# Kernel tuning notes

Measured on AMD Instinct MI355X. Metric: run time of the kernel, lower is better.

Reference implementation:

```python
import jax, jax.numpy as jnp
import numpy as np

N_NODES = 100000
N_EDGES = 3200000
IN_F = 256
OUT_F = 256


def setup_inputs() -> dict:
    key = jax.random.key(0)
    k1, k2, k3, k4, k5 = jax.random.split(key, 5)
    input_ = jax.random.normal(k1, (N_NODES, IN_F), dtype=jnp.float32)
    edge_src = jax.random.randint(k2, (N_EDGES,), 0, N_NODES, dtype=jnp.int64)
    edge_dst = jax.random.randint(k3, (N_EDGES,), 0, N_NODES, dtype=jnp.int64)
    edge_val = jax.random.uniform(k4, (N_EDGES,), dtype=jnp.float32)
    stdv = 1.0 / np.sqrt(OUT_F)
    weight = jax.random.uniform(k5, (IN_F, OUT_F), dtype=jnp.float32,
                                minval=-stdv, maxval=stdv)
    return {"input_": input_, "edge_src": edge_src, "edge_dst": edge_dst,
            "edge_val": edge_val, "weight": weight}


def reference(input_, edge_src, edge_dst, edge_val, weight):
    # neighbor = spmm(adj, input_): adj in COO form (dst, src, val)
    gathered = edge_val[:, None] * input_[edge_src]          # [E, F]
    neighbor = jax.ops.segment_sum(gathered, edge_dst,
                                   num_segments=N_NODES)     # [N, F]
    ft_input = input_ @ weight                               # [N, O]
    ft_neighbor = neighbor @ weight                          # [N, O]
    return jnp.concatenate([ft_input, ft_neighbor], axis=1)  # [N, 2*O]
```

## Files before the change

kernel.cpp:

```cpp
#include <hip/hip_runtime.h>
#include <hip/hip_fp16.h>

#define N_NODES 100000
#define N_EDGES 3200000
#define F 256

#define BM 64
#define BN 256
#define BK 32

#define MAX_DEG 80
#define INIT_NB ((N_NODES + 255) / 256)
#define EDGE_NB4 (N_EDGES / 1024)
#define GEMM_NB ((N_NODES + BM - 1) / BM)
#define FUSED_NB (GEMM_NB + EDGE_NB4)

typedef __attribute__((ext_vector_type(8))) short short8;
typedef __attribute__((ext_vector_type(4))) float f32x4;

__device__ inline unsigned short f2bf(float f) {
    unsigned int u = __float_as_uint(f);
    unsigned int r = (u + 0x7fffu + ((u >> 16) & 1u)) >> 16;
    return (unsigned short)r;
}

__device__ inline float bf2f(unsigned short b) {
    return __uint_as_float(((unsigned int)b) << 16);
}

__device__ inline unsigned int pack_rec(int src, float val) {
    __half h = __float2half(val);
    unsigned short hb = *reinterpret_cast<unsigned short*>(&h);
    return ((unsigned int)src << 15) | (unsigned int)hb;
}

__device__ inline int rec_src(unsigned int p) { return (int)(p >> 15); }

__device__ inline float rec_val(unsigned int p) {
    unsigned short hb = (unsigned short)(p & 0x7FFFu);
    __half h = *reinterpret_cast<__half*>(&hb);
    return __half2float(h);
}

__global__ __launch_bounds__(256)
void init_kernel(const float* __restrict__ W, unsigned short* __restrict__ Wt,
                 int* __restrict__ counts) {
    const int idx = blockIdx.x * 256 + threadIdx.x;
    if (idx < N_NODES) counts[idx] = 0;
    if (idx < 256 * 256) {
        const int n = idx >> 8;
        const int k = idx & 255;
        Wt[n * 256 + k] = f2bf(W[k * 256 + n]);
    }
}

__global__ __launch_bounds__(256, 3)
void gemm_bucket_kernel(const float* __restrict__ A,
                        const unsigned short* __restrict__ Wt,
                        float* __restrict__ out,
                        unsigned short* __restrict__ ftb,
                        const int* __restrict__ src,
                        const int* __restrict__ dst,
                        const float* __restrict__ val,
                        int* __restrict__ counts,
                        unsigned int* __restrict__ recs)
{
    const int bid = blockIdx.x;

    if (bid % 3 != 0) {
        const int ebid = 2 * (bid / 3) + (bid % 3) - 1;
        const int e0 = (ebid * 256 + threadIdx.x) * 4;
        const int4   s = *(const int4*)(src + e0);
        const int4   d = *(const int4*)(dst + e0);
        const float4 v = *(const float4*)(val + e0);
        const int r0 = atomicAdd(&counts[d.x], 1);
        const int r1 = atomicAdd(&counts[d.y], 1);
        const int r2 = atomicAdd(&counts[d.z], 1);
        const int r3 = atomicAdd(&counts[d.w], 1);
        if (r0 < MAX_DEG) recs[d.x * MAX_DEG + r0] = pack_rec(s.x, v.x);
        if (r1 < MAX_DEG) recs[d.y * MAX_DEG + r1] = pack_rec(s.y, v.y);
        if (r2 < MAX_DEG) recs[d.z * MAX_DEG + r2] = pack_rec(s.z, v.z);
        if (r3 < MAX_DEG) recs[d.w * MAX_DEG + r3] = pack_rec(s.w, v.w);
        return;
    }

    const int tid   = threadIdx.x;
    const int lane  = tid & 63;
    const int wave  = tid >> 6;
    const int waveM = wave >> 1;
    const int waveN = wave & 1;
    const int rowBase = (bid / 3) * BM;

    const int quad = lane >> 4;
    const int l16  = lane & 15;

    f32x4 acc[2][8];
#pragma unroll
    for (int i = 0; i < 2; i++)
#pragma unroll
        for (int j = 0; j < 8; j++) acc[i][j] = (f32x4)0.0f;

    const int row0 = rowBase + waveM * 32 + l16;
    const int row1 = row0 + 16;
    const bool ok0 = row0 < N_NODES;
    const bool ok1 = row1 < N_NODES;
    const float* pa0 = A + (size_t)row0 * 256 + quad * 8;
    const float* pa1 = A + (size_t)row1 * 256 + quad * 8;
    const unsigned short* pb = Wt + (size_t)(waveN * 128 + l16) * 256 + quad * 8;

    for (int kt = 0; kt < 8; kt++) {
        const int k0 = kt * BK;

        short8 af[2];
#pragma unroll
        for (int i = 0; i < 2; i++) {
            const float* pa = (i == 0) ? pa0 : pa1;
            const bool ok = (i == 0) ? ok0 : ok1;
            short8 av;
            if (ok) {
                const float4 f0 = *(const float4*)(pa + k0);
                const float4 f1 = *(const float4*)(pa + k0 + 4);
                av[0] = (short)f2bf(f0.x); av[1] = (short)f2bf(f0.y);
                av[2] = (short)f2bf(f0.z); av[3] = (short)f2bf(f0.w);
                av[4] = (short)f2bf(f1.x); av[5] = (short)f2bf(f1.y);
                av[6] = (short)f2bf(f1.z); av[7] = (short)f2bf(f1.w);
            } else {
                av = (short8)0;
            }
            af[i] = av;
        }

        short8 bfr[8];
#pragma unroll
        for (int j = 0; j < 8; j++)
            bfr[j] = *(const short8*)(pb + (size_t)(j * 16) * 256 + k0);

#pragma unroll
        for (int i = 0; i < 2; i++)
#pragma unroll
            for (int j = 0; j < 8; j++)
                acc[i][j] = __builtin_amdgcn_mfma_f32_16x16x32_bf16(
                    bfr[j], af[i], acc[i][j], 0, 0, 0);
    }

#pragma unroll
    for (int i = 0; i < 2; i++) {
        const int row = rowBase + waveM * 32 + i * 16 + l16;
        if (row < N_NODES) {
#pragma unroll
            for (int j = 0; j < 8; j++) {
                const int col = waveN * 128 + j * 16 + quad * 4;
                f32x4 v = acc[i][j];
                *(f32x4*)(out + (size_t)row * 512 + col) = v;
                unsigned int p0 = ((unsigned int)f2bf(v[1]) << 16) | f2bf(v[0]);
                unsigned int p1 = ((unsigned int)f2bf(v[3]) << 16) | f2bf(v[2]);
                *(uint2*)(ftb + (size_t)row * 256 + col) = make_uint2(p0, p1);
            }
        }
    }
}

__global__ __launch_bounds__(256)
void gather_kernel(const int* __restrict__ counts,
                   const unsigned int* __restrict__ recs,
                   const unsigned short* __restrict__ ftb,
                   float* __restrict__ out)
{
    const int n = blockIdx.x * 4 + (threadIdx.x >> 6);
    if (n >= N_NODES) return;
    const int lane = threadIdx.x & 63;

    int len = counts[n];
    if (len > MAX_DEG) len = MAX_DEG;
    const unsigned int* rp = recs + (size_t)n * MAX_DEG;

    float ax = 0.f, ay = 0.f, az = 0.f, aw = 0.f;

    int e = 0;

    if (e + 7 < len) {
        unsigned int r[8];
#pragma unroll
        for (int q = 0; q < 8; q++) r[q] = rp[e + q];
        while (true) {
            const int en = e + 8;
            const bool moreN = (en + 7 < len);
            unsigned int rn[8];
            if (moreN) {
#pragma unroll
                for (int q = 0; q < 8; q++) rn[q] = rp[en + q];
            }
            ushort4 u[8];
#pragma unroll
            for (int q = 0; q < 8; q++)
                u[q] = *(const ushort4*)(ftb + (size_t)rec_src(r[q]) * 256 + lane * 4);
#pragma unroll
            for (int q = 0; q < 8; q++) {
                const float v = rec_val(r[q]);
                ax += v * bf2f(u[q].x); ay += v * bf2f(u[q].y);
                az += v * bf2f(u[q].z); aw += v * bf2f(u[q].w);
            }
            e = en;
            if (!moreN) break;
#pragma unroll
            for (int q = 0; q < 8; q++) r[q] = rn[q];
        }
    }

    for (; e + 3 < len; e += 4) {
        unsigned int r0 = rp[e];
        unsigned int r1 = rp[e + 1];
        unsigned int r2 = rp[e + 2];
        unsigned int r3 = rp[e + 3];
        ushort4 u0 = *(const ushort4*)(ftb + (size_t)rec_src(r0) * 256 + lane * 4);
        ushort4 u1 = *(const ushort4*)(ftb + (size_t)rec_src(r1) * 256 + lane * 4);
        ushort4 u2 = *(const ushort4*)(ftb + (size_t)rec_src(r2) * 256 + lane * 4);
        ushort4 u3 = *(const ushort4*)(ftb + (size_t)rec_src(r3) * 256 + lane * 4);
        const float v0 = rec_val(r0);
        const float v1 = rec_val(r1);
        const float v2 = rec_val(r2);
        const float v3 = rec_val(r3);
        ax += v0 * bf2f(u0.x); ay += v0 * bf2f(u0.y);
        az += v0 * bf2f(u0.z); aw += v0 * bf2f(u0.w);
        ax += v1 * bf2f(u1.x); ay += v1 * bf2f(u1.y);
        az += v1 * bf2f(u1.z); aw += v1 * bf2f(u1.w);
        ax += v2 * bf2f(u2.x); ay += v2 * bf2f(u2.y);
        az += v2 * bf2f(u2.z); aw += v2 * bf2f(u2.w);
        ax += v3 * bf2f(u3.x); ay += v3 * bf2f(u3.y);
        az += v3 * bf2f(u3.z); aw += v3 * bf2f(u3.w);
    }
    for (; e < len; e++) {
        unsigned int r0 = rp[e];
        ushort4 u0 = *(const ushort4*)(ftb + (size_t)rec_src(r0) * 256 + lane * 4);
        const float v0 = rec_val(r0);
        ax += v0 * bf2f(u0.x); ay += v0 * bf2f(u0.y);
        az += v0 * bf2f(u0.z); aw += v0 * bf2f(u0.w);
    }

    float4 res = make_float4(ax, ay, az, aw);
    *(float4*)(out + (size_t)n * 512 + 256 + lane * 4) = res;
}

extern "C" void kernel_launch(void* const* d_in, const int* in_sizes, int n_in,
                              void* d_out, int out_size, void* d_ws, size_t ws_size,
                              hipStream_t stream)
{
    const float* input = (const float*)d_in[0];
    const int*   esrc  = (const int*)d_in[1];
    const int*   edst  = (const int*)d_in[2];
    const float* eval  = (const float*)d_in[3];
    const float* W     = (const float*)d_in[4];
    float* out = (float*)d_out;

    char* ws = (char*)d_ws;
    unsigned short* Wt  = (unsigned short*)(ws);
    int* counts         = (int*)(ws + 131072);
    unsigned int* recs  = (unsigned int*)(ws + 532480);
    unsigned short* ftb = (unsigned short*)(ws + 32532480);

    init_kernel<<<INIT_NB, 256, 0, stream>>>(W, Wt, counts);

    gemm_bucket_kernel<<<FUSED_NB, 256, 0, stream>>>(
        input, Wt, out, ftb, esrc, edst, eval, counts, recs);

    gather_kernel<<<(N_NODES + 3) / 4, 256, 0, stream>>>(counts, recs, ftb, out);
}
```

Before: 710.2 us.

## Stage converted A tile through double-buffered LDS shared across waves

Each thread now loads and converts one 8-element slice of the A tile to bf16 once and writes it into a double-buffered shared-memory tile. All waves then read their MFMA operands from LDS, where before each wave pair redundantly loaded and converted the same rows from global memory. The next k-tile is prefetched while the current one is consumed, at the cost of a block barrier per k-step and 8KB of LDS, which may lower occupancy for the fused edge-bucketing blocks.

```diff
diff --git a/kernel.cpp b/kernel.cpp
--- a/kernel.cpp
+++ b/kernel.cpp
@@ -65,6 +65,8 @@
                         int* __restrict__ counts,
                         unsigned int* __restrict__ recs)
 {
+    __shared__ unsigned short As[2][BM * BK];
+
     const int bid = blockIdx.x;
 
     if (bid % 3 != 0) {
@@ -91,49 +93,56 @@
     const int waveN = wave & 1;
     const int rowBase = (bid / 3) * BM;
 
+    const int sr = tid >> 2;
+    const int sk = (tid & 3) * 8;
     const int quad = lane >> 4;
     const int l16  = lane & 15;
 
+    const int  grow = rowBase + sr;
+    const bool gok  = grow < N_NODES;
+    const float* pa = A + (size_t)grow * 256 + sk;
+    const unsigned short* pb = Wt + (size_t)(waveN * 128 + l16) * 256 + quad * 8;
+
     f32x4 acc[2][8];
 #pragma unroll
     for (int i = 0; i < 2; i++)
 #pragma unroll
         for (int j = 0; j < 8; j++) acc[i][j] = (f32x4)0.0f;
 
-    const int row0 = rowBase + waveM * 32 + l16;
-    const int row1 = row0 + 16;
-    const bool ok0 = row0 < N_NODES;
-    const bool ok1 = row1 < N_NODES;
-    const float* pa0 = A + (size_t)row0 * 256 + quad * 8;
-    const float* pa1 = A + (size_t)row1 * 256 + quad * 8;
-    const unsigned short* pb = Wt + (size_t)(waveN * 128 + l16) * 256 + quad * 8;
-
+#define STAGE_A(buf, kt)                                                     \
+    {                                                                        \
+        short8 av;                                                           \
+        if (gok) {                                                           \
+            const float4 f0 = *(const float4*)(pa + (kt) * BK);              \
+            const float4 f1 = *(const float4*)(pa + (kt) * BK + 4);          \
+            av[0] = (short)f2bf(f0.x); av[1] = (short)f2bf(f0.y);            \
+            av[2] = (short)f2bf(f0.z); av[3] = (short)f2bf(f0.w);            \
+            av[4] = (short)f2bf(f1.x); av[5] = (short)f2bf(f1.y);            \
+            av[6] = (short)f2bf(f1.z); av[7] = (short)f2bf(f1.w);            \
+        } else {                                                             \
+            av = (short8)0;                                                  \
+        }                                                                    \
+        *(short8*)(&As[buf][sr * BK + sk]) = av;                             \
+    }
+
+    STAGE_A(0, 0);
+    __syncthreads();
+
+#pragma unroll
     for (int kt = 0; kt < 8; kt++) {
+        const int cur = kt & 1;
+        if (kt < 7) STAGE_A(cur ^ 1, kt + 1);
+
         const int k0 = kt * BK;
-
-        short8 af[2];
-#pragma unroll
-        for (int i = 0; i < 2; i++) {
-            const float* pa = (i == 0) ? pa0 : pa1;
-            const bool ok = (i == 0) ? ok0 : ok1;
-            short8 av;
-            if (ok) {
-                const float4 f0 = *(const float4*)(pa + k0);
-                const float4 f1 = *(const float4*)(pa + k0 + 4);
-                av[0] = (short)f2bf(f0.x); av[1] = (short)f2bf(f0.y);
-                av[2] = (short)f2bf(f0.z); av[3] = (short)f2bf(f0.w);
-                av[4] = (short)f2bf(f1.x); av[5] = (short)f2bf(f1.y);
-                av[6] = (short)f2bf(f1.z); av[7] = (short)f2bf(f1.w);
-            } else {
-                av = (short8)0;
-            }
-            af[i] = av;
-        }
-
         short8 bfr[8];
 #pragma unroll
         for (int j = 0; j < 8; j++)
             bfr[j] = *(const short8*)(pb + (size_t)(j * 16) * 256 + k0);
+
+        short8 af[2];
+#pragma unroll
+        for (int i = 0; i < 2; i++)
+            af[i] = *(const short8*)(&As[cur][(waveM * 32 + i * 16 + l16) * BK + quad * 8]);
 
 #pragma unroll
         for (int i = 0; i < 2; i++)
@@ -141,7 +150,10 @@
             for (int j = 0; j < 8; j++)
                 acc[i][j] = __builtin_amdgcn_mfma_f32_16x16x32_bf16(
                     bfr[j], af[i], acc[i][j], 0, 0, 0);
-    }
+
+        __syncthreads();
+    }
+#undef STAGE_A
 
 #pragma unroll
     for (int i = 0; i < 2; i++) {
```

New measurement: 666.7 us. 1.07x faster.
